# Kernel optimization log

Measured on AMD Instinct MI355X. Metric: run time of the kernel, lower is better.

Reference implementation:

```python
import jax, jax.numpy as jnp
import numpy as np
import math

B, S, D = 4, 4096, 2048
HEAD_DIM = 128  # dim_model // head_nums = 2048 // 16
DEPTH = 12


def setup_inputs() -> dict:
    key = jax.random.key(0)
    ks = jax.random.split(key, 8)
    std = 0.1
    return {
        "x": jax.random.normal(ks[0], (B, S, D), dtype=jnp.float32),
        "WQ": jax.random.normal(ks[1], (D, 2 * HEAD_DIM), dtype=jnp.float32) * (D ** -0.5),
        "WK": jax.random.normal(ks[2], (D, 2 * HEAD_DIM), dtype=jnp.float32) * (D ** -0.5),
        "WV": jax.random.normal(ks[3], (D, 2 * HEAD_DIM), dtype=jnp.float32) * (D ** -0.5),
        "lambda_q1": jax.random.normal(ks[4], (HEAD_DIM,), dtype=jnp.float32) * std,
        "lambda_q2": jax.random.normal(ks[5], (HEAD_DIM,), dtype=jnp.float32) * std,
        "lambda_k1": jax.random.normal(ks[6], (HEAD_DIM,), dtype=jnp.float32) * std,
        "lambda_k2": jax.random.normal(ks[7], (HEAD_DIM,), dtype=jnp.float32) * std,
    }


def reference(x, WQ, WK, WV, lambda_q1, lambda_q2, lambda_k1, lambda_k2):
    scale = HEAD_DIM ** -0.5
    lambda_init = 0.8 - 0.6 * math.exp(-0.3 * DEPTH)

    q = x @ WQ                      # [B, S, 2*hd]
    k = x @ WK
    v = x @ WV                      # [B, S, 2*hd]
    q1, q2 = q[..., :HEAD_DIM], q[..., HEAD_DIM:]
    k1, k2 = k[..., :HEAD_DIM], k[..., HEAD_DIM:]

    a1 = jnp.einsum("bqd,bkd->bqk", q1, k1) * scale  # [B, S, S]
    a2 = jnp.einsum("bqd,bkd->bqk", q2, k2) * scale

    lambda_1 = jnp.exp(jnp.sum(lambda_q1 * lambda_k1))
    lambda_2 = jnp.exp(jnp.sum(lambda_q2 * lambda_k2))
    lam = lambda_1 + lambda_2 + lambda_init

    attn = jax.nn.softmax(a1, axis=-1) - lam * jax.nn.softmax(a2, axis=-1)
    return jnp.einsum("bqk,bkd->bqd", attn, v)  # [B, S, 2*hd]
```

## Files before the change

kernel.cpp:

```cpp
#include <hip/hip_runtime.h>
#include <stdint.h>

typedef unsigned short u16;
typedef __attribute__((ext_vector_type(4))) float f32x4;
typedef __attribute__((ext_vector_type(16))) float f32x16;
typedef __attribute__((ext_vector_type(8))) short s16x8;
typedef __attribute__((ext_vector_type(8))) __bf16 bf16x8;
typedef __attribute__((ext_vector_type(8))) unsigned short u16x8;
typedef __attribute__((ext_vector_type(4))) unsigned short u16x4;
typedef __attribute__((ext_vector_type(4))) uint32_t u32x4;

__device__ __forceinline__ f32x4 mfma16(s16x8 a, s16x8 b, f32x4 c) {
  return __builtin_amdgcn_mfma_f32_16x16x32_bf16(
      __builtin_bit_cast(bf16x8, a), __builtin_bit_cast(bf16x8, b), c, 0, 0, 0);
}
__device__ __forceinline__ f32x16 mfma32(s16x8 a, s16x8 b, f32x16 c) {
  return __builtin_amdgcn_mfma_f32_32x32x16_bf16(
      __builtin_bit_cast(bf16x8, a), __builtin_bit_cast(bf16x8, b), c, 0, 0, 0);
}

__device__ __forceinline__ void gl_lds16(const u16* g, u16* l) {
  __builtin_amdgcn_global_load_lds(
      (const __attribute__((address_space(1))) void*)g,
      (__attribute__((address_space(3))) void*)l, 16, 0, 0);
}

__device__ __forceinline__ u16 bf16rne(float f) {
  uint32_t u = __builtin_bit_cast(uint32_t, f);
  u += 0x7fffu + ((u >> 16) & 1u);
  return (u16)(u >> 16);
}

__global__ void cast_x_kernel(const float* __restrict__ x, u16* __restrict__ xb) {
  size_t i = ((size_t)blockIdx.x * 256 + threadIdx.x) * 8;
  f32x4 a = *(const f32x4*)(x + i);
  f32x4 b = *(const f32x4*)(x + i + 4);
  u16x8 o;
#pragma unroll
  for (int j = 0; j < 4; ++j) { o[j] = bf16rne(a[j]); o[4 + j] = bf16rne(b[j]); }
  *(u16x8*)(xb + i) = o;
}

__global__ void cast_w_kernel(const float* __restrict__ WQ, const float* __restrict__ WK,
                              const float* __restrict__ WV, u16* __restrict__ Wt, float qscale) {
  int i = blockIdx.x * 256 + threadIdx.x;
  int r = i >> 11, k = i & 2047;
  int sel = r >> 8, c = r & 255;
  const float* W = (sel == 0) ? WQ : (sel == 1) ? WK : WV;
  float v = W[(size_t)k * 256 + c];
  if (sel == 0) v *= qscale;
  Wt[i] = bf16rne(v);
}

__global__ __launch_bounds__(256) void proj_gemm(const u16* __restrict__ xb, const u16* __restrict__ Wt,
                                                 u16* __restrict__ Qb, u16* __restrict__ Kb,
                                                 u16* __restrict__ Vt) {
  const int bid = blockIdx.x;
  const int xcd = bid & 7, j = bid >> 3;
  const int m0 = (xcd * 16 + (j / 6)) * 128;
  const int n0 = (j % 6) * 128;
  const int tid = threadIdx.x, lane = tid & 63, w = tid >> 6;
  const int ln = lane & 15, quad = lane >> 4;
  const int wm = w & 1, wn = w >> 1;
  __shared__ __align__(16) u16 As[128 * 32];
  __shared__ __align__(16) u16 Bs[128 * 32];
  f32x4 acc[4][4];
#pragma unroll
  for (int i = 0; i < 4; ++i)
#pragma unroll
    for (int jj = 0; jj < 4; ++jj) acc[i][jj] = f32x4{0.f, 0.f, 0.f, 0.f};

  for (int kk = 0; kk < 2048; kk += 32) {
    __syncthreads();
#pragma unroll
    for (int i = 0; i < 2; ++i) {
      int p = tid + i * 256;
      int row = p >> 2, cg = (p & 3) ^ (row & 3);
      gl_lds16(xb + (size_t)(m0 + row) * 2048 + kk + cg * 8, As + (size_t)(p - lane) * 8);
      gl_lds16(Wt + (size_t)(n0 + row) * 2048 + kk + cg * 8, Bs + (size_t)(p - lane) * 8);
    }
    __syncthreads();
    s16x8 a[4];
#pragma unroll
    for (int mt = 0; mt < 4; ++mt) {
      int r = wm * 64 + mt * 16 + ln;
      a[mt] = *(const s16x8*)(As + r * 32 + ((quad ^ (r & 3)) * 8));
    }
#pragma unroll
    for (int nt = 0; nt < 4; ++nt) {
      int r = wn * 64 + nt * 16 + ln;
      s16x8 bf = *(const s16x8*)(Bs + r * 32 + ((quad ^ (r & 3)) * 8));
#pragma unroll
      for (int mt = 0; mt < 4; ++mt) acc[mt][nt] = mfma16(a[mt], bf, acc[mt][nt]);
    }
  }
#pragma unroll
  for (int mt = 0; mt < 4; ++mt)
#pragma unroll
    for (int nt = 0; nt < 4; ++nt) {
      int row0 = m0 + wm * 64 + mt * 16 + quad * 4;
      int col = n0 + wn * 64 + nt * 16 + ln;
      int sel = col >> 8, c = col & 255;
      u16x4 vv;
#pragma unroll
      for (int jj = 0; jj < 4; ++jj) vv[jj] = bf16rne(acc[mt][nt][jj]);
      if (sel == 2) {
        int b = row0 >> 12, s = row0 & 4095;
        *(u16x4*)(Vt + (size_t)b * 1048576 + (size_t)c * 4096 + s) = vv;
      } else {
        u16* dst = (sel == 0) ? Qb : Kb;
#pragma unroll
        for (int jj = 0; jj < 4; ++jj) dst[(size_t)(row0 + jj) * 256 + c] = vv[jj];
      }
    }
}

__global__ void lam_kernel(const float* __restrict__ lq1, const float* __restrict__ lq2,
                           const float* __restrict__ lk1, const float* __restrict__ lk2,
                           float* __restrict__ lamp) {
  int t = threadIdx.x;
  float d1 = lq1[t] * lk1[t] + lq1[t + 64] * lk1[t + 64];
  float d2 = lq2[t] * lk2[t] + lq2[t + 64] * lk2[t + 64];
#pragma unroll
  for (int off = 32; off; off >>= 1) {
    d1 += __shfl_xor(d1, off);
    d2 += __shfl_xor(d2, off);
  }
  if (t == 0) *lamp = expf(d1) + expf(d2) + (0.8f - 0.6f * expf(-3.6f));
}

__global__ __launch_bounds__(256, 2) void attn_kernel(const u16* __restrict__ Qb,
                                                      const u16* __restrict__ Kb,
                                                      const u16* __restrict__ Vt,
                                                      const float* __restrict__ lamp,
                                                      float* __restrict__ out) {
  const int bid = blockIdx.x;
  const int xcd = bid & 7;
  const int b = xcd >> 1;
  const int qt = ((bid >> 3) << 1) + (xcd & 1);
  const int tid = threadIdx.x, lane = tid & 63, w = tid >> 6;
  const int l5 = lane & 31, lh = lane >> 5;
  const int m = w & 1, kt = w >> 1;

  __shared__ __align__(16) char smem[68096];
  u16* Ks = (u16*)smem;
  u16* Vs = (u16*)(smem + 32768);
  float* buf0 = (float*)smem;
  float* buf1 = (float*)(smem + 33792);
  float* ls = (float*)(smem + 67584);

  s16x8 bq[8];
  {
    const u16* qp = Qb + ((size_t)(b * 4096 + qt * 32 + l5)) * 256 + m * 128 + lh * 8;
#pragma unroll
    for (int s = 0; s < 8; ++s) bq[s] = *(const s16x8*)(qp + s * 16);
  }

  f32x16 O[8];
#pragma unroll
  for (int ct = 0; ct < 8; ++ct)
#pragma unroll
    for (int r = 0; r < 16; ++r) O[ct][r] = 0.f;
  float l_run = 0.f;

  const u16* Kg0 = Kb + ((size_t)b * 4096) * 256;
  const u16* Vg0 = Vt + (size_t)b * 1048576;

  for (int kb = 0; kb < 4096; kb += 64) {
    __syncthreads();
#pragma unroll
    for (int i = 0; i < 8; ++i) {
      int p = tid + i * 256;
      int row = p >> 5, c = p & 31;
      int cg = (c & 16) | ((c ^ row) & 15);
      gl_lds16(Kg0 + (size_t)(kb + row) * 256 + cg * 8, Ks + (size_t)(p - lane) * 8);
    }
#pragma unroll
    for (int i = 0; i < 8; ++i) {
      int p = tid + i * 256;
      int row = p >> 3, c = p & 7;
      int cg = c ^ (row & 7);
      gl_lds16(Vg0 + (size_t)row * 4096 + kb + cg * 8, Vs + (size_t)(p - lane) * 8);
    }
    __syncthreads();

    f32x16 Sa, Sb;
#pragma unroll
    for (int r = 0; r < 16; ++r) { Sa[r] = 0.f; Sb[r] = 0.f; }
#pragma unroll
    for (int s = 0; s < 8; s += 2) {
      int row = kt * 32 + l5;
      int c0 = m * 16 + s * 2 + lh;
      int c1 = m * 16 + (s + 1) * 2 + lh;
      s16x8 a0 = *(const s16x8*)(Ks + row * 256 + (((c0 & 16) | ((c0 ^ row) & 15))) * 8);
      s16x8 a1 = *(const s16x8*)(Ks + row * 256 + (((c1 & 16) | ((c1 ^ row) & 15))) * 8);
      Sa = mfma32(a0, bq[s], Sa);
      Sb = mfma32(a1, bq[s + 1], Sb);
    }

    uint32_t P[8];
#pragma unroll
    for (int d = 0; d < 8; ++d) {
      float p0 = exp2f(Sa[2 * d] + Sb[2 * d]);
      float p1 = exp2f(Sa[2 * d + 1] + Sb[2 * d + 1]);
      l_run += p0 + p1;
      P[d] = (uint32_t)bf16rne(p0) | ((uint32_t)bf16rne(p1) << 16);
    }
    uint32_t X[8];
#pragma unroll
    for (int d = 0; d < 8; ++d) X[d] = (uint32_t)__shfl_xor((int)P[d], 32);

#pragma unroll
    for (int ks = 0; ks < 2; ++ks) {
      u32x4 fd;
      fd[0] = lh ? X[ks * 4 + 2] : P[ks * 4 + 0];
      fd[1] = lh ? X[ks * 4 + 3] : P[ks * 4 + 1];
      fd[2] = lh ? P[ks * 4 + 2] : X[ks * 4 + 0];
      fd[3] = lh ? P[ks * 4 + 3] : X[ks * 4 + 1];
      s16x8 pf = __builtin_bit_cast(s16x8, fd);
      int c = (kt * 32 + ks * 16) / 8 + lh;
#pragma unroll
      for (int ct = 0; ct < 8; ++ct) {
        int row = ct * 32 + l5;
        s16x8 vf = *(const s16x8*)(Vs + row * 64 + ((c ^ (row & 7)) * 8));
        O[ct] = mfma32(vf, pf, O[ct]);
      }
    }
  }

  float lam = *lamp;
  l_run += __shfl_xor(l_run, 32);
  __syncthreads();
  if (lane < 32) ls[(m * 2 + kt) * 32 + l5] = l_run;
  float* bufm = m ? buf1 : buf0;
  if (kt == 1) {
#pragma unroll
    for (int ct = 0; ct < 8; ++ct)
#pragma unroll
      for (int r = 0; r < 16; ++r) {
        int vcol = ct * 32 + (r & 3) + 8 * (r >> 2) + 4 * lh;
        bufm[vcol * 33 + l5] = O[ct][r];
      }
  }
  __syncthreads();
  if (kt == 0) {
    float linv = 1.f / (ls[(m * 2) * 32 + l5] + ls[(m * 2 + 1) * 32 + l5]);
#pragma unroll
    for (int ct = 0; ct < 8; ++ct)
#pragma unroll
      for (int r = 0; r < 16; ++r) {
        int vcol = ct * 32 + (r & 3) + 8 * (r >> 2) + 4 * lh;
        bufm[vcol * 33 + l5] = (O[ct][r] + bufm[vcol * 33 + l5]) * linv;
      }
  }
  __syncthreads();
  float* og = out + ((size_t)(b * 4096 + qt * 32)) * 256;
#pragma unroll
  for (int j2 = 0; j2 < 32; ++j2) {
    float v = buf0[tid * 33 + j2] - lam * buf1[tid * 33 + j2];
    og[(size_t)j2 * 256 + tid] = v;
  }
}

extern "C" void kernel_launch(void* const* d_in, const int* in_sizes, int n_in,
                              void* d_out, int out_size, void* d_ws, size_t ws_size,
                              hipStream_t stream) {
  (void)in_sizes; (void)n_in; (void)out_size; (void)ws_size;
  const float* x   = (const float*)d_in[0];
  const float* WQ  = (const float*)d_in[1];
  const float* WK  = (const float*)d_in[2];
  const float* WV  = (const float*)d_in[3];
  const float* lq1 = (const float*)d_in[4];
  const float* lq2 = (const float*)d_in[5];
  const float* lk1 = (const float*)d_in[6];
  const float* lk2 = (const float*)d_in[7];
  float* out = (float*)d_out;

  char* ws = (char*)d_ws;
  u16* xb = (u16*)ws;   ws += (size_t)16384 * 2048 * 2;
  u16* Wt = (u16*)ws;   ws += (size_t)768 * 2048 * 2;
  u16* Qb = (u16*)ws;   ws += (size_t)16384 * 256 * 2;
  u16* Kb = (u16*)ws;   ws += (size_t)16384 * 256 * 2;
  u16* Vt = (u16*)ws;   ws += (size_t)16384 * 256 * 2;
  float* lamp = (float*)ws;

  const float qscale = 0.0883883476f * 1.44269504f;

  hipLaunchKernelGGL(cast_x_kernel, dim3(16384), dim3(256), 0, stream, x, xb);
  hipLaunchKernelGGL(cast_w_kernel, dim3(6144), dim3(256), 0, stream, WQ, WK, WV, Wt, qscale);
  hipLaunchKernelGGL(proj_gemm, dim3(768), dim3(256), 0, stream, xb, Wt, Qb, Kb, Vt);
  hipLaunchKernelGGL(lam_kernel, dim3(1), dim3(64), 0, stream, lq1, lq2, lk1, lk2, lamp);
  hipLaunchKernelGGL(attn_kernel, dim3(512), dim3(256), 0, stream, Qb, Kb, Vt, lamp, out);
}
```

Measured before the change: 430.3 us.

## Double-buffer V in LDS, load K straight to registers, fuse lambda into attention

The attention loop now loads K fragments directly from global memory into registers, so K no longer goes through LDS. V tiles are double-buffered in LDS with a new XOR swizzle, and the next tile is prefetched while the current one is used, leaving one barrier per iteration instead of two. The exponent uses the hardware exp2 intrinsic, and P is packed to bf16 by truncation with a byte permute instead of round-to-nearest-even, which slightly changes numerics. The lambda computation moves into the attention epilogue, removing a separate kernel launch.

```diff
diff --git a/kernel.cpp b/kernel.cpp
--- a/kernel.cpp
+++ b/kernel.cpp
@@ -115,24 +115,13 @@
     }
 }
 
-__global__ void lam_kernel(const float* __restrict__ lq1, const float* __restrict__ lq2,
-                           const float* __restrict__ lk1, const float* __restrict__ lk2,
-                           float* __restrict__ lamp) {
-  int t = threadIdx.x;
-  float d1 = lq1[t] * lk1[t] + lq1[t + 64] * lk1[t + 64];
-  float d2 = lq2[t] * lk2[t] + lq2[t + 64] * lk2[t + 64];
-#pragma unroll
-  for (int off = 32; off; off >>= 1) {
-    d1 += __shfl_xor(d1, off);
-    d2 += __shfl_xor(d2, off);
-  }
-  if (t == 0) *lamp = expf(d1) + expf(d2) + (0.8f - 0.6f * expf(-3.6f));
-}
-
 __global__ __launch_bounds__(256, 2) void attn_kernel(const u16* __restrict__ Qb,
                                                       const u16* __restrict__ Kb,
                                                       const u16* __restrict__ Vt,
-                                                      const float* __restrict__ lamp,
+                                                      const float* __restrict__ lq1,
+                                                      const float* __restrict__ lq2,
+                                                      const float* __restrict__ lk1,
+                                                      const float* __restrict__ lk2,
                                                       float* __restrict__ out) {
   const int bid = blockIdx.x;
   const int xcd = bid & 7;
@@ -142,12 +131,13 @@
   const int l5 = lane & 31, lh = lane >> 5;
   const int m = w & 1, kt = w >> 1;
 
-  __shared__ __align__(16) char smem[68096];
-  u16* Ks = (u16*)smem;
-  u16* Vs = (u16*)(smem + 32768);
+  __shared__ __align__(16) char smem[68608];
+  u16* Vs0 = (u16*)smem;
+  u16* Vs1 = (u16*)(smem + 32768);
   float* buf0 = (float*)smem;
   float* buf1 = (float*)(smem + 33792);
   float* ls = (float*)(smem + 67584);
+  float* lamS = (float*)(smem + 68096);
 
   s16x8 bq[8];
   {
@@ -163,48 +153,55 @@
     for (int r = 0; r < 16; ++r) O[ct][r] = 0.f;
   float l_run = 0.f;
 
-  const u16* Kg0 = Kb + ((size_t)b * 4096) * 256;
+  const u16* Kg = Kb + ((size_t)(b * 4096 + kt * 32 + l5)) * 256 + m * 128 + lh * 8;
   const u16* Vg0 = Vt + (size_t)b * 1048576;
 
-  for (int kb = 0; kb < 4096; kb += 64) {
+#pragma unroll
+  for (int i = 0; i < 8; ++i) {
+    int p = tid + i * 256;
+    int row = p >> 3, cs = p & 7;
+    int g = (cs ^ row ^ (row >> 3)) & 7;
+    gl_lds16(Vg0 + (size_t)row * 4096 + g * 8, Vs0 + (size_t)(p - lane) * 8);
+  }
+
+  for (int it = 0; it < 64; ++it) {
     __syncthreads();
-#pragma unroll
-    for (int i = 0; i < 8; ++i) {
-      int p = tid + i * 256;
-      int row = p >> 5, c = p & 31;
-      int cg = (c & 16) | ((c ^ row) & 15);
-      gl_lds16(Kg0 + (size_t)(kb + row) * 256 + cg * 8, Ks + (size_t)(p - lane) * 8);
-    }
-#pragma unroll
-    for (int i = 0; i < 8; ++i) {
-      int p = tid + i * 256;
-      int row = p >> 3, c = p & 7;
-      int cg = c ^ (row & 7);
-      gl_lds16(Vg0 + (size_t)row * 4096 + kb + cg * 8, Vs + (size_t)(p - lane) * 8);
-    }
-    __syncthreads();
+    u16* Vcur = (it & 1) ? Vs1 : Vs0;
+    u16* Vnxt = (it & 1) ? Vs0 : Vs1;
+
+    const u16* kp = Kg + (size_t)it * 64 * 256;
+    s16x8 ak[8];
+#pragma unroll
+    for (int s = 0; s < 8; ++s) ak[s] = *(const s16x8*)(kp + s * 16);
+
+    if (it + 1 < 64) {
+      const u16* vg = Vg0 + (it + 1) * 64;
+#pragma unroll
+      for (int i = 0; i < 8; ++i) {
+        int p = tid + i * 256;
+        int row = p >> 3, cs = p & 7;
+        int g = (cs ^ row ^ (row >> 3)) & 7;
+        gl_lds16(vg + (size_t)row * 4096 + g * 8, Vnxt + (size_t)(p - lane) * 8);
+      }
+    }
 
     f32x16 Sa, Sb;
 #pragma unroll
     for (int r = 0; r < 16; ++r) { Sa[r] = 0.f; Sb[r] = 0.f; }
 #pragma unroll
     for (int s = 0; s < 8; s += 2) {
-      int row = kt * 32 + l5;
-      int c0 = m * 16 + s * 2 + lh;
-      int c1 = m * 16 + (s + 1) * 2 + lh;
-      s16x8 a0 = *(const s16x8*)(Ks + row * 256 + (((c0 & 16) | ((c0 ^ row) & 15))) * 8);
-      s16x8 a1 = *(const s16x8*)(Ks + row * 256 + (((c1 & 16) | ((c1 ^ row) & 15))) * 8);
-      Sa = mfma32(a0, bq[s], Sa);
-      Sb = mfma32(a1, bq[s + 1], Sb);
+      Sa = mfma32(ak[s], bq[s], Sa);
+      Sb = mfma32(ak[s + 1], bq[s + 1], Sb);
     }
 
     uint32_t P[8];
 #pragma unroll
     for (int d = 0; d < 8; ++d) {
-      float p0 = exp2f(Sa[2 * d] + Sb[2 * d]);
-      float p1 = exp2f(Sa[2 * d + 1] + Sb[2 * d + 1]);
+      float p0 = __builtin_amdgcn_exp2f(Sa[2 * d] + Sb[2 * d]);
+      float p1 = __builtin_amdgcn_exp2f(Sa[2 * d + 1] + Sb[2 * d + 1]);
       l_run += p0 + p1;
-      P[d] = (uint32_t)bf16rne(p0) | ((uint32_t)bf16rne(p1) << 16);
+      P[d] = __builtin_amdgcn_perm(__builtin_bit_cast(uint32_t, p1),
+                                   __builtin_bit_cast(uint32_t, p0), 0x07060302u);
     }
     uint32_t X[8];
 #pragma unroll
@@ -218,20 +215,30 @@
       fd[2] = lh ? P[ks * 4 + 2] : X[ks * 4 + 0];
       fd[3] = lh ? P[ks * 4 + 3] : X[ks * 4 + 1];
       s16x8 pf = __builtin_bit_cast(s16x8, fd);
-      int c = (kt * 32 + ks * 16) / 8 + lh;
+      int c = kt * 4 + ks * 2 + lh;
 #pragma unroll
       for (int ct = 0; ct < 8; ++ct) {
         int row = ct * 32 + l5;
-        s16x8 vf = *(const s16x8*)(Vs + row * 64 + ((c ^ (row & 7)) * 8));
+        int slot = (c ^ row ^ (row >> 3)) & 7;
+        s16x8 vf = *(const s16x8*)(Vcur + row * 64 + slot * 8);
         O[ct] = mfma32(vf, pf, O[ct]);
       }
     }
   }
 
-  float lam = *lamp;
   l_run += __shfl_xor(l_run, 32);
   __syncthreads();
   if (lane < 32) ls[(m * 2 + kt) * 32 + l5] = l_run;
+  if (w == 0) {
+    float d1 = lq1[lane] * lk1[lane] + lq1[lane + 64] * lk1[lane + 64];
+    float d2 = lq2[lane] * lk2[lane] + lq2[lane + 64] * lk2[lane + 64];
+#pragma unroll
+    for (int off = 32; off; off >>= 1) {
+      d1 += __shfl_xor(d1, off);
+      d2 += __shfl_xor(d2, off);
+    }
+    if (lane == 0) lamS[0] = expf(d1) + expf(d2) + (0.8f - 0.6f * expf(-3.6f));
+  }
   float* bufm = m ? buf1 : buf0;
   if (kt == 1) {
 #pragma unroll
@@ -254,6 +261,7 @@
       }
   }
   __syncthreads();
+  float lam = lamS[0];
   float* og = out + ((size_t)(b * 4096 + qt * 32)) * 256;
 #pragma unroll
   for (int j2 = 0; j2 < 32; ++j2) {
@@ -282,13 +290,12 @@
   u16* Qb = (u16*)ws;   ws += (size_t)16384 * 256 * 2;
   u16* Kb = (u16*)ws;   ws += (size_t)16384 * 256 * 2;
   u16* Vt = (u16*)ws;   ws += (size_t)16384 * 256 * 2;
-  float* lamp = (float*)ws;
 
   const float qscale = 0.0883883476f * 1.44269504f;
 
   hipLaunchKernelGGL(cast_x_kernel, dim3(16384), dim3(256), 0, stream, x, xb);
   hipLaunchKernelGGL(cast_w_kernel, dim3(6144), dim3(256), 0, stream, WQ, WK, WV, Wt, qscale);
   hipLaunchKernelGGL(proj_gemm, dim3(768), dim3(256), 0, stream, xb, Wt, Qb, Kb, Vt);
-  hipLaunchKernelGGL(lam_kernel, dim3(1), dim3(64), 0, stream, lq1, lq2, lk1, lk2, lamp);
-  hipLaunchKernelGGL(attn_kernel, dim3(512), dim3(256), 0, stream, Qb, Kb, Vt, lamp, out);
-}
+  hipLaunchKernelGGL(attn_kernel, dim3(512), dim3(256), 0, stream, Qb, Kb, Vt,
+                     lq1, lq2, lk1, lk2, out);
+}
```

After: 479.6 us. 1.11x slower.
